# Kernel tuning notes

Hardware: AMD Instinct MI355X
Metric: run time of the kernel (lower is better)

Reference implementation:

```python
import jax, jax.numpy as jnp
import numpy as np

B, C, S = 256, 1024, 14   # batch, channels, spatial (frozen by y.view(b,c,14,14))
C2 = 15                   # channels2 in the module
CAT = C // 2 * 3 + C2     # 1551 = 15 + 512 + 1024
EPS = 1e-5


def _conv(x, w, b, groups, pad):
    out = jax.lax.conv_general_dilated(
        x, w, window_strides=(1, 1), padding=((pad, pad), (pad, pad)),
        dimension_numbers=('NCHW', 'OIHW', 'NCHW'), feature_group_count=groups)
    return out + b[None, :, None, None]


def _bn(x, gamma, beta):
    # training-mode BatchNorm2d: biased batch stats over (N,H,W)
    m = x.mean((0, 2, 3), keepdims=True)
    v = x.var((0, 2, 3), keepdims=True)
    return (x - m) * jax.lax.rsqrt(v + EPS) * gamma[None, :, None, None] + beta[None, :, None, None]


def setup_inputs() -> dict:
    key = jax.random.key(0)
    ks = jax.random.split(key, 16)
    r = C2 // 7  # = 2
    inp = {
        'y': jax.random.normal(ks[0], (B, C2, S * S), jnp.float32),
        'x': jax.random.normal(ks[1], (B, C, S, S), jnp.float32),
        'fc1_w': jax.random.normal(ks[2], (r, C2), jnp.float32) * 0.2,
        'fc2_w': jax.random.normal(ks[3], (C2, r), jnp.float32) * 0.2,
        'conv_w': jax.random.normal(ks[4], (C // 2, C, 1, 1), jnp.float32) * 0.03,
        'conv_b': jnp.zeros((C // 2,), jnp.float32),
        'dconv_w': jax.random.normal(ks[5], (C, 1, 3, 3), jnp.float32) * 0.2,
        'dconv_b': jnp.zeros((C,), jnp.float32),
        'dw1_w': jax.random.normal(ks[6], (CAT, 1, 3, 3), jnp.float32) * 0.2,
        'dw1_b': jnp.zeros((CAT,), jnp.float32),
        'pw1_w': jax.random.normal(ks[7], (C // 2, CAT, 1, 1), jnp.float32) * 0.03,
        'pw1_b': jnp.zeros((C // 2,), jnp.float32),
        'gamma': jnp.ones((C // 2,), jnp.float32),
        'beta': jnp.zeros((C // 2,), jnp.float32),
        'n': 0,
    }
    return inp


def reference(y, x, fc1_w, fc2_w, conv_w, conv_b, dconv_w, dconv_b,
              dw1_w, dw1_b, pw1_w, pw1_b, gamma, beta, n):
    b = y.shape[0]
    y4 = y.reshape(b, C2, S, S)
    # SE block on the 15 sub-channels
    g = y4.mean((2, 3))                              # (b, 15) global avg pool
    h = jax.nn.relu(g @ fc1_w.T) @ fc2_w.T           # (b, 15)
    y1 = y4 * jax.nn.sigmoid(h)[:, :, None, None]
    # depthwise conv on x, then per-(b,c) row covariance of the 14x14 map
    x1 = _conv(x, dconv_w, dconv_b, C, 1)            # (b, C, 14, 14)
    x2 = jax.lax.stop_gradient(x1)                   # .detach() in the original
    xc = x2 - x2.mean(-1, keepdims=True)             # np.cov: rows=vars, cols=obs
    cov = jnp.einsum('bcik,bcjk->bcij', xc, xc) / (S - 1)
    z = _conv(cov, conv_w, conv_b, 1, 0)             # 1x1 conv C -> C//2
    z = jax.nn.sigmoid(_bn(z, gamma, beta))
    for _ in range(n):                               # n=0 at these shapes
        y1 = jax.image.resize(y1, (y1.shape[0], y1.shape[1], y1.shape[2] * 2, y1.shape[3] * 2), 'bilinear')
    cat = jnp.concatenate([y1, z, x], axis=1)        # (b, 1551, 14, 14)
    o = _conv(cat, dw1_w, dw1_b, CAT, 1)             # depthwise 3x3
    o = _conv(o, pw1_w, pw1_b, 1, 0)                 # pointwise 1x1 -> C//2
    return jax.nn.relu(_bn(o, gamma, beta))
```

## Files before the change

### kernel.cpp

```cpp
#include <hip/hip_runtime.h>

typedef unsigned int u32;
typedef unsigned short u16;
typedef __attribute__((ext_vector_type(8))) short bf16x8;
typedef __attribute__((ext_vector_type(4))) float f32x4;
typedef __attribute__((ext_vector_type(4))) u32 u32x4;

#define EPSBN 1e-5f

#define GLDS16(gp, lp) __builtin_amdgcn_global_load_lds( \
    (const __attribute__((address_space(1))) u32*)(gp), \
    (__attribute__((address_space(3))) u32*)(lp), 16, 0, 0)

#define OFF_ADW    0ull
#define OFF_COVT   0ull
#define OFF_S      160563200ull
#define OFF_WBZ    160578560ull
#define OFF_WBP    161627136ull
#define OFF_STATSZ 163265536ull
#define OFF_STATSO 163269632ull
#define OFF_SCZ    163273728ull
#define OFF_SHZ    163275776ull
#define OFF_SCO    163277824ull
#define OFF_SHO    163279872ull

static __device__ __forceinline__ float bf2f(u16 h){
  u32 u = ((u32)h) << 16; float f; __builtin_memcpy(&f, &u, 4); return f;
}
static __device__ __forceinline__ u16 f2bf(float f){
  u32 u; __builtin_memcpy(&u, &f, 4);
  u = (u + 0x7fffu + ((u >> 16) & 1u)) >> 16;
  return (u16)u;
}
static __device__ __forceinline__ u32 pk2bf(float lo, float hi){
  u32 r;
  asm("v_cvt_pk_bf16_f32 %0, %1, %2" : "=v"(r) : "v"(lo), "v"(hi));
  return r;
}

__global__ __launch_bounds__(64) void se_kernel(const float* __restrict__ y,
    const float* __restrict__ fc1, const float* __restrict__ fc2, float* __restrict__ sse){
  __shared__ float g[15];
  __shared__ float t[2];
  int b = blockIdx.x, l = threadIdx.x;
  for (int c = 0; c < 15; ++c){
    float p = 0.f;
    for (int k = l; k < 196; k += 64) p += y[((size_t)b*15 + c)*196 + k];
    p += __shfl_xor(p, 32); p += __shfl_xor(p, 16); p += __shfl_xor(p, 8);
    p += __shfl_xor(p, 4);  p += __shfl_xor(p, 2);  p += __shfl_xor(p, 1);
    if (l == 0) g[c] = p * (1.f/196.f);
  }
  __syncthreads();
  if (l < 2){
    float a = 0.f;
    for (int c = 0; c < 15; ++c) a += g[c] * fc1[l*15 + c];
    t[l] = fmaxf(a, 0.f);
  }
  __syncthreads();
  if (l < 15){
    float h = t[0]*fc2[l*2] + t[1]*fc2[l*2+1];
    sse[b*15 + l] = 1.f / (1.f + __expf(-h));
  }
}

__global__ void wconv_kernel(const float* __restrict__ cw, const float* __restrict__ pw,
                             u16* __restrict__ wbz, u16* __restrict__ wbp){
  u32 stride = gridDim.x * blockDim.x;
  for (u32 i = blockIdx.x*blockDim.x + threadIdx.x; i < 524288u; i += stride)
    wbz[i] = f2bf(cw[i]);
  for (u32 i = blockIdx.x*blockDim.x + threadIdx.x; i < 819200u; i += stride){
    u32 n = i / 1600u, k = i - n*1600u;
    wbp[i] = f2bf(k < 1551u ? pw[(size_t)n*1551 + k] : 0.f);
  }
}

__global__ __launch_bounds__(256,2) void cov_kernel(const float* __restrict__ x,
    const float* __restrict__ dcw, const float* __restrict__ dcb, u16* __restrict__ covT){
  __shared__ __align__(16) float xs[2*3136];
  __shared__ __align__(16) u32 xcb[16*132];
  __shared__ __align__(16) u32 covL32[32*210];
  __shared__ float wls[64][9];
  __shared__ float wlb[64];

  int tid = threadIdx.x;
  int c0 = blockIdx.x * 64, b = blockIdx.y;
  const float* xbase = x + ((size_t)b*1024 + c0)*196;

  #pragma unroll
  for (int i = 0; i < 3; ++i){
    int s = tid + i*256;
    GLDS16(xbase + s*4, xs + s*4);
  }
  if (tid < 16){ int s = tid + 768; GLDS16(xbase + s*4, xs + s*4); }

  for (int i = tid; i < 576; i += 256) wls[i/9][i%9] = dcw[(size_t)(c0 + i/9)*9 + (i%9)];
  if (tid < 64) wlb[tid] = dcb[c0 + tid];

  for (int sg = 0; sg < 4; ++sg){
    u32 xo = (u32)(sg & 1) * 3136u;
    asm volatile("s_waitcnt vmcnt(0)" ::: "memory");
    __builtin_amdgcn_s_barrier();
    asm volatile("" ::: "memory");

    {
      int c = tid >> 4, i = tid & 15;
      int cg = sg*16 + c;
      u32 q[8];
      #pragma unroll
      for (int j = 0; j < 8; ++j) q[j] = 0u;
      if (i < 14){
        float wr[9];
        #pragma unroll
        for (int qq = 0; qq < 9; ++qq) wr[qq] = wls[cg][qq];
        float topm = (i > 0) ? 1.f : 0.f, botm = (i < 13) ? 1.f : 0.f;
        wr[0] *= topm; wr[1] *= topm; wr[2] *= topm;
        wr[6] *= botm; wr[7] *= botm; wr[8] *= botm;
        float bb = wlb[cg];
        float rr[3][16];
        #pragma unroll
        for (int d = 0; d < 3; ++d){
          rr[d][0] = 0.f; rr[d][15] = 0.f;
          int rowr = i + d - 1;
          rowr = rowr < 0 ? 0 : (rowr > 13 ? 13 : rowr);
          const float* src = &xs[xo + c*196 + rowr*14];
          #pragma unroll
          for (int j = 0; j < 7; ++j)
            *(float2*)&rr[d][1 + 2*j] = *(const float2*)&src[2*j];
        }
        float ov[14];
        #pragma unroll
        for (int k = 0; k < 14; ++k){
          float a = bb;
          #pragma unroll
          for (int dy = 0; dy < 3; ++dy)
            #pragma unroll
            for (int dx = 0; dx < 3; ++dx)
              a += wr[dy*3+dx] * rr[dy][k + dx];
          ov[k] = a;
        }
        float mean = 0.f;
        #pragma unroll
        for (int k = 0; k < 14; ++k) mean += ov[k];
        mean *= (1.f/14.f);
        #pragma unroll
        for (int j = 0; j < 7; ++j)
          q[j] = pk2bf(ov[2*j] - mean, ov[2*j+1] - mean);
      }
      u32x4 q0 = {q[0], q[1], q[2], q[3]};
      u32x4 q1 = {q[4], q[5], q[6], q[7]};
      *(u32x4*)&xcb[c*132 + i*8]     = q0;
      *(u32x4*)&xcb[c*132 + i*8 + 4] = q1;
    }
    __builtin_amdgcn_s_barrier();
    if (sg < 3){
      const float* nsrc = xbase + (size_t)(sg+1)*3136;
      u32 xo2 = xo ^ 3136u;
      #pragma unroll
      for (int i = 0; i < 3; ++i){
        int s = tid + i*256;
        GLDS16(nsrc + s*4, xs + xo2 + s*4);
      }
      if (tid < 16){ int s = tid + 768; GLDS16(nsrc + s*4, xs + xo2 + s*4); }
    }

    {
      int w = tid >> 6, l = tid & 63, lr = l & 15, lq = l >> 4;
      #pragma unroll
      for (int pp = 0; pp < 2; ++pp){
        int clo = w*4 + 2*pp;
        bf16x8 alo = {0,0,0,0,0,0,0,0}, ahi = {0,0,0,0,0,0,0,0};
        if (lq < 2){
          alo = *(const bf16x8*)&xcb[clo*132 + lr*8 + lq*4];
          ahi = *(const bf16x8*)&xcb[(clo+1)*132 + lr*8 + lq*4];
        }
        f32x4 dlo = {0.f,0.f,0.f,0.f}, dhi = {0.f,0.f,0.f,0.f};
        dlo = __builtin_amdgcn_mfma_f32_16x16x32_bf16(alo, alo, dlo, 0, 0, 0);
        dhi = __builtin_amdgcn_mfma_f32_16x16x32_bf16(ahi, ahi, dhi, 0, 0, 0);
        if (lr < 14){
          int cp = sg*8 + w*2 + pp;
          #pragma unroll
          for (int r = 0; r < 4; ++r){
            int rowi = lq*4 + r;
            if (rowi < 14){
              u32 vv = pk2bf(dlo[r] * (1.f/13.f), dhi[r] * (1.f/13.f));
              covL32[cp*210 + rowi*14 + lr] = vv;
            }
          }
        }
      }
    }
  }
  __syncthreads();

  for (int i = tid; i < 1568; i += 256){
    int g = i & 7, ij = i >> 3;
    u32x4 v;
    v.x = covL32[(g*4+0)*210 + ij];
    v.y = covL32[(g*4+1)*210 + ij];
    v.z = covL32[(g*4+2)*210 + ij];
    v.w = covL32[(g*4+3)*210 + ij];
    *(u32x4*)(covT + ((size_t)(b*196 + ij)*1024 + c0 + g*8)) = v;
  }
}

__global__ __launch_bounds__(256,5) void adw_kernel(
    const float* __restrict__ y, const float* __restrict__ sse,
    const u16* __restrict__ zT, const float* __restrict__ scz, const float* __restrict__ shz,
    const float* __restrict__ x, const float* __restrict__ dw1w, const float* __restrict__ dw1b,
    u16* __restrict__ Adw){
  __shared__ __align__(16) float ms[32*202];
  __shared__ float wd[32][9];
  __shared__ float bd[32];
  int tid = threadIdx.x;
  int cc0 = blockIdx.x * 32, b = blockIdx.y;

  for (int i = tid; i < 288; i += 256){
    int c = i / 9, q = i - c*9;
    int cc = cc0 + c;
    wd[c][q] = (cc < 1551) ? dw1w[(size_t)cc*9 + q] : 0.f;
  }
  if (tid < 32) bd[tid] = (cc0 + tid < 1551) ? dw1b[cc0 + tid] : 0.f;

  if (cc0 < 15){
    int ny = 15;
    for (int i = tid; i < ny*196; i += 256){
      u32 c = (u32)i / 196u, p = (u32)i - c*196u;
      ms[c*202u + p] = y[((size_t)b*15 + c)*196 + p] * sse[b*15 + c];
    }
  }
  {
    int zs = cc0 > 15 ? cc0 : 15;
    int ze = cc0 + 32 < 527 ? cc0 + 32 : 527;
    if (zs < ze){
      int nz = ze - zs, lbase = zs - cc0, obase = zs - 15;
      const u16* zrow = zT + (size_t)obase*50176 + (size_t)b*196;
      for (int i = tid; i < nz*98; i += 256){
        u32 oo = (u32)i / 98u, pp = (u32)i - oo*98u;
        u32 v = *(const u32*)(zrow + (size_t)oo*50176 + pp*2u);
        int o = obase + (int)oo;
        float s = scz[o], h = shz[o];
        float v0 = bf2f((u16)(v & 0xffffu)) * s + h;
        float v1 = bf2f((u16)(v >> 16))     * s + h;
        v0 = 1.f / (1.f + __expf(-v0));
        v1 = 1.f / (1.f + __expf(-v1));
        float2 fv = {v0, v1};
        *(float2*)&ms[(u32)(lbase + (int)oo)*202u + pp*2u] = fv;
      }
    }
  }
  {
    int xs_ = cc0 > 527 ? cc0 : 527;
    int xe = cc0 + 32 < 1551 ? cc0 + 32 : 1551;
    if (xs_ < xe){
      int nx = xe - xs_, lbase = xs_ - cc0, cxs = xs_ - 527;
      const float4* xg = (const float4*)(x + ((size_t)b*1024 + cxs)*196);
      for (int i = tid; i < nx*49; i += 256){
        float4 v = xg[i];
        u32 c = (u32)i / 49u, p4 = (u32)i - c*49u;
        float* dst = &ms[(u32)(lbase + (int)c)*202u + p4*4u];
        float2 lo = {v.x, v.y}, hi = {v.z, v.w};
        *(float2*)dst = lo;
        *(float2*)(dst + 2) = hi;
      }
    }
  }
  {
    int ps = cc0 > 1551 ? cc0 : 1551;
    int pe = cc0 + 32;
    if (ps < pe){
      int np = pe - ps, lbase = ps - cc0;
      for (int i = tid; i < np*196; i += 256){
        u32 c = (u32)i / 196u, p = (u32)i - c*196u;
        ms[(u32)(lbase + (int)c)*202u + p] = 0.f;
      }
    }
  }
  __syncthreads();

  for (int t = tid; t < 448; t += 256){
    int cc = t & 31, i = t >> 5;
    float wr[9];
    #pragma unroll
    for (int qq = 0; qq < 9; ++qq) wr[qq] = wd[cc][qq];
    float topm = (i > 0) ? 1.f : 0.f, botm = (i < 13) ? 1.f : 0.f;
    wr[0] *= topm; wr[1] *= topm; wr[2] *= topm;
    wr[6] *= botm; wr[7] *= botm; wr[8] *= botm;
    float bb = bd[cc];
    float rr[3][16];
    #pragma unroll
    for (int d = 0; d < 3; ++d){
      rr[d][0] = 0.f; rr[d][15] = 0.f;
      int rowr = i + d - 1;
      rowr = rowr < 0 ? 0 : (rowr > 13 ? 13 : rowr);
      const float* src = &ms[cc*202 + rowr*14];
      #pragma unroll
      for (int j = 0; j < 7; ++j)
        *(float2*)&rr[d][1 + 2*j] = *(const float2*)&src[2*j];
    }
    size_t obase = ((size_t)b*196 + i*14) * 1600 + cc0 + cc;
    #pragma unroll
    for (int k = 0; k < 14; ++k){
      float a = bb;
      #pragma unroll
      for (int dy = 0; dy < 3; ++dy)
        #pragma unroll
        for (int dx = 0; dx < 3; ++dx)
          a += wr[dy*3+dx] * rr[dy][k + dx];
      Adw[obase + (size_t)k*1600] = f2bf(a);
    }
  }
}

template<int MODE>
__global__ __launch_bounds__(256,2) void gemm_kernel(
    const u16* __restrict__ A, const u16* __restrict__ Bw,
    const float* __restrict__ bias, void* __restrict__ outp,
    float* __restrict__ stats, int K){
  __shared__ __align__(16) u16 lds[32768];

  int tid = threadIdx.x;
  int w = tid >> 6, l = tid & 63;
  int wm = w >> 1, wn = w & 1;
  int lr = l & 15, lq = l >> 4;
  u32 g = blockIdx.x;
  u32 lin = (g & 7u) * 196u + (g >> 3);
  int n0 = (int)(lin & 3u) * 128;
  int m0 = (int)(lin >> 2) * 128;

  f32x4 acc[4][4] = {};
  int kTiles = K >> 6;

  const u16* Abase = A  + (size_t)m0*K;
  const u16* Bbase = Bw + (size_t)n0*K;

  #pragma unroll
  for (int i = 0; i < 4; ++i){
    int s = tid + i*256;
    int row = s >> 3, c8 = s & 7, sc = c8 ^ (row & 7);
    GLDS16(Abase + (size_t)row*K + sc*8, lds + s*8);
    GLDS16(Bbase + (size_t)row*K + sc*8, lds + 8192 + s*8);
  }

  for (int kt = 0; kt < kTiles; ++kt){
    u32 bufo = (u32)(kt & 1) * 16384u;
    if (kt > 0) __builtin_amdgcn_s_barrier();
    if (kt + 1 < kTiles){
      u32 nbufo = bufo ^ 16384u;
      #pragma unroll
      for (int i = 0; i < 4; ++i){
        int s = tid + i*256;
        int row = s >> 3, c8 = s & 7, sc = c8 ^ (row & 7);
        GLDS16(Abase + (size_t)row*K + (kt+1)*64 + sc*8, lds + nbufo + s*8);
        GLDS16(Bbase + (size_t)row*K + (kt+1)*64 + sc*8, lds + nbufo + 8192 + s*8);
      }
      asm volatile("s_waitcnt vmcnt(8)" ::: "memory");
    } else {
      asm volatile("s_waitcnt vmcnt(0)" ::: "memory");
    }
    __builtin_amdgcn_s_barrier();
    asm volatile("" ::: "memory");
    const u16* Ac = lds + bufo;
    const u16* Bc = lds + bufo + 8192;
    #pragma unroll
    for (int ks = 0; ks < 2; ++ks){
      bf16x8 af[4], bfv[4];
      #pragma unroll
      for (int mi = 0; mi < 4; ++mi){
        int row = wm*64 + mi*16 + lr;
        int q = (ks*4 + lq) ^ (row & 7);
        af[mi] = *(const bf16x8*)(Ac + row*64 + q*8);
      }
      #pragma unroll
      for (int ni = 0; ni < 4; ++ni){
        int row = wn*64 + ni*16 + lr;
        int q = (ks*4 + lq) ^ (row & 7);
        bfv[ni] = *(const bf16x8*)(Bc + row*64 + q*8);
      }
      #pragma unroll
      for (int mi = 0; mi < 4; ++mi)
        #pragma unroll
        for (int ni = 0; ni < 4; ++ni)
          acc[mi][ni] = __builtin_amdgcn_mfma_f32_16x16x32_bf16(af[mi], bfv[ni], acc[mi][ni], 0, 0, 0);
    }
  }
  __syncthreads();

  #pragma unroll
  for (int ni = 0; ni < 4; ++ni){
    int col = n0 + wn*64 + ni*16 + lr;
    float bb = bias[col];
    float s1 = 0.f, s2 = 0.f;
    #pragma unroll
    for (int mi = 0; mi < 4; ++mi)
      #pragma unroll
      for (int r = 0; r < 4; ++r){
        float v = acc[mi][ni][r] + bb;
        acc[mi][ni][r] = v;
        s1 += v; s2 += v*v;
      }
    s1 += __shfl_xor(s1, 16); s1 += __shfl_xor(s1, 32);
    s2 += __shfl_xor(s2, 16); s2 += __shfl_xor(s2, 32);
    if (lq == 0){
      atomicAdd(&stats[col], s1);
      atomicAdd(&stats[512 + col], s2);
    }
  }

  float* eb = (float*)lds;
  #pragma unroll
  for (int rnd = 0; rnd < 2; ++rnd){
    if (wm == rnd){
      float* e = eb + wn * (64*65);
      #pragma unroll
      for (int mi = 0; mi < 4; ++mi)
        #pragma unroll
        for (int ni = 0; ni < 4; ++ni)
          #pragma unroll
          for (int r = 0; r < 4; ++r)
            e[(mi*16 + lq*4 + r)*65 + ni*16 + lr] = acc[mi][ni][r];
      int m = m0 + wm*64 + l;
      if (MODE == 0){
        u16* ob = (u16*)outp + (size_t)(n0 + wn*64)*50176 + m;
        #pragma unroll 8
        for (int no = 0; no < 64; ++no)
          ob[(size_t)no*50176] = f2bf(e[l*65 + no]);
      } else {
        u32 bq = (u32)m / 196u;
        u32 ij = (u32)m - bq*196u;
        float* ob = (float*)outp + ((size_t)bq*512 + n0 + wn*64)*196 + ij;
        #pragma unroll 8
        for (int no = 0; no < 64; ++no)
          ob[(size_t)no*196] = e[l*65 + no];
      }
    }
    __syncthreads();
  }
}

__global__ void bnprep_kernel(const float* __restrict__ stats, const float* __restrict__ gamma,
    const float* __restrict__ beta, float* __restrict__ sc, float* __restrict__ sh){
  int o = threadIdx.x;
  float m = stats[o] * (1.f/50176.f);
  float v = stats[512+o] * (1.f/50176.f) - m*m;
  float inv = rsqrtf(v + EPSBN);
  float g = gamma[o] * inv;
  sc[o] = g;
  sh[o] = beta[o] - m*g;
}

__global__ void final_kernel(float4* __restrict__ o4, const float* __restrict__ sc,
                             const float* __restrict__ sh){
  u32 stride = gridDim.x * blockDim.x;
  for (u32 i = blockIdx.x*blockDim.x + threadIdx.x; i < 6422528u; i += stride){
    u32 oc = (i / 49u) & 511u;
    float s = sc[oc], t = sh[oc];
    float4 v = o4[i];
    v.x = fmaxf(fmaf(v.x, s, t), 0.f);
    v.y = fmaxf(fmaf(v.y, s, t), 0.f);
    v.z = fmaxf(fmaf(v.z, s, t), 0.f);
    v.w = fmaxf(fmaf(v.w, s, t), 0.f);
    o4[i] = v;
  }
}

extern "C" void kernel_launch(void* const* d_in, const int* in_sizes, int n_in,
                              void* d_out, int out_size, void* d_ws, size_t ws_size,
                              hipStream_t stream){
  (void)in_sizes; (void)n_in; (void)out_size; (void)ws_size;
  const float* y      = (const float*)d_in[0];
  const float* x      = (const float*)d_in[1];
  const float* fc1    = (const float*)d_in[2];
  const float* fc2    = (const float*)d_in[3];
  const float* convw  = (const float*)d_in[4];
  const float* convb  = (const float*)d_in[5];
  const float* dconvw = (const float*)d_in[6];
  const float* dconvb = (const float*)d_in[7];
  const float* dw1w   = (const float*)d_in[8];
  const float* dw1b   = (const float*)d_in[9];
  const float* pw1w   = (const float*)d_in[10];
  const float* pw1b   = (const float*)d_in[11];
  const float* gamma  = (const float*)d_in[12];
  const float* beta   = (const float*)d_in[13];

  char* ws = (char*)d_ws;
  u16* covT   = (u16*)(ws + OFF_COVT);
  u16* Adw    = (u16*)(ws + OFF_ADW);
  float* sse  = (float*)(ws + OFF_S);
  u16* wbz    = (u16*)(ws + OFF_WBZ);
  u16* wbp    = (u16*)(ws + OFF_WBP);
  float* statsZ = (float*)(ws + OFF_STATSZ);
  float* statsO = (float*)(ws + OFF_STATSO);
  float* scz  = (float*)(ws + OFF_SCZ);
  float* shz  = (float*)(ws + OFF_SHZ);
  float* sco  = (float*)(ws + OFF_SCO);
  float* sho  = (float*)(ws + OFF_SHO);
  u16* zT     = (u16*)d_out;
  float* outf = (float*)d_out;

  hipMemsetAsync(statsZ, 0, 8192, stream);
  se_kernel<<<256, 64, 0, stream>>>(y, fc1, fc2, sse);
  wconv_kernel<<<2048, 256, 0, stream>>>(convw, pw1w, wbz, wbp);
  cov_kernel<<<dim3(16, 256), 256, 0, stream>>>(x, dconvw, dconvb, covT);
  gemm_kernel<0><<<1568, 256, 0, stream>>>(covT, wbz, convb, (void*)zT, statsZ, 1024);
  bnprep_kernel<<<1, 512, 0, stream>>>(statsZ, gamma, beta, scz, shz);
  adw_kernel<<<dim3(50, 256), 256, 0, stream>>>(y, sse, zT, scz, shz, x, dw1w, dw1b, Adw);
  gemm_kernel<1><<<1568, 256, 0, stream>>>(Adw, wbp, pw1b, (void*)outf, statsO, 1600);
  bnprep_kernel<<<1, 512, 0, stream>>>(statsO, gamma, beta, sco, sho);
  final_kernel<<<8192, 256, 0, stream>>>((float4*)outf, sco, sho);
}
```

Baseline: 485.6 us.

## Exploit covariance symmetry: compute only upper-triangle entries through the z GEMM

Since each 14x14 covariance is symmetric, the cov kernel writes only the 105 upper-triangle entries per (b,c), and the first GEMM runs over M=256*105 instead of 256*196. The GEMM weights off-diagonal rows twice in the BatchNorm statistics so the batch mean and variance stay exact. The adw kernel expands the z output back to the full 14x14 map through a lookup table. This cuts the first GEMM's FLOPs and the covT/zT memory traffic by nearly half, in exchange for scalar u16 gathers in adw instead of paired loads, plus extra per-block table setup.

```diff
diff --git a/kernel.cpp b/kernel.cpp
--- a/kernel.cpp
+++ b/kernel.cpp
@@ -81,6 +81,7 @@
   __shared__ __align__(16) u32 covL32[32*210];
   __shared__ float wls[64][9];
   __shared__ float wlb[64];
+  __shared__ u16 tij[112];
 
   int tid = threadIdx.x;
   int c0 = blockIdx.x * 64, b = blockIdx.y;
@@ -95,6 +96,13 @@
 
   for (int i = tid; i < 576; i += 256) wls[i/9][i%9] = dcw[(size_t)(c0 + i/9)*9 + (i%9)];
   if (tid < 64) wlb[tid] = dcb[c0 + tid];
+  if (tid < 196){
+    int ii = tid / 14, jj = tid - ii*14;
+    if (ii <= jj){
+      int t = 13*ii - (ii*(ii-1))/2 + jj;
+      tij[t] = (u16)tid;
+    }
+  }
 
   for (int sg = 0; sg < 4; ++sg){
     u32 xo = (u32)(sg & 1) * 3136u;
@@ -192,14 +200,15 @@
   }
   __syncthreads();
 
-  for (int i = tid; i < 1568; i += 256){
-    int g = i & 7, ij = i >> 3;
+  for (int i = tid; i < 840; i += 256){
+    int g = i & 7, t = i >> 3;
+    int ij = tij[t];
     u32x4 v;
     v.x = covL32[(g*4+0)*210 + ij];
     v.y = covL32[(g*4+1)*210 + ij];
     v.z = covL32[(g*4+2)*210 + ij];
     v.w = covL32[(g*4+3)*210 + ij];
-    *(u32x4*)(covT + ((size_t)(b*196 + ij)*1024 + c0 + g*8)) = v;
+    *(u32x4*)(covT + ((size_t)(b*105 + t)*1024 + c0 + g*8)) = v;
   }
 }
 
@@ -211,8 +220,16 @@
   __shared__ __align__(16) float ms[32*202];
   __shared__ float wd[32][9];
   __shared__ float bd[32];
+  __shared__ u16 ttab[196];
   int tid = threadIdx.x;
   int cc0 = blockIdx.x * 32, b = blockIdx.y;
+
+  if (tid < 196){
+    int ii = tid / 14, jj = tid - ii*14;
+    int im = ii < jj ? ii : jj, jm = ii < jj ? jj : ii;
+    ttab[tid] = (u16)(13*im - (im*(im-1))/2 + jm);
+  }
+  __syncthreads();
 
   for (int i = tid; i < 288; i += 256){
     int c = i / 9, q = i - c*9;
@@ -233,18 +250,14 @@
     int ze = cc0 + 32 < 527 ? cc0 + 32 : 527;
     if (zs < ze){
       int nz = ze - zs, lbase = zs - cc0, obase = zs - 15;
-      const u16* zrow = zT + (size_t)obase*50176 + (size_t)b*196;
-      for (int i = tid; i < nz*98; i += 256){
-        u32 oo = (u32)i / 98u, pp = (u32)i - oo*98u;
-        u32 v = *(const u32*)(zrow + (size_t)oo*50176 + pp*2u);
+      const u16* zb = zT + (size_t)obase*26880 + (size_t)b*105;
+      for (int i = tid; i < nz*196; i += 256){
+        u32 oo = (u32)i / 196u, p = (u32)i - oo*196u;
+        float v = bf2f(zb[(size_t)oo*26880 + ttab[p]]);
         int o = obase + (int)oo;
-        float s = scz[o], h = shz[o];
-        float v0 = bf2f((u16)(v & 0xffffu)) * s + h;
-        float v1 = bf2f((u16)(v >> 16))     * s + h;
-        v0 = 1.f / (1.f + __expf(-v0));
-        v1 = 1.f / (1.f + __expf(-v1));
-        float2 fv = {v0, v1};
-        *(float2*)&ms[(u32)(lbase + (int)oo)*202u + pp*2u] = fv;
+        v = v * scz[o] + shz[o];
+        v = 1.f / (1.f + __expf(-v));
+        ms[(u32)(lbase + (int)oo)*202u + p] = v;
       }
     }
   }
@@ -323,7 +336,8 @@
   int wm = w >> 1, wn = w & 1;
   int lr = l & 15, lq = l >> 4;
   u32 g = blockIdx.x;
-  u32 lin = (g & 7u) * 196u + (g >> 3);
+  u32 per = gridDim.x >> 3;
+  u32 lin = (g & 7u) * per + (g >> 3);
   int n0 = (int)(lin & 3u) * 128;
   int m0 = (int)(lin >> 2) * 128;
 
@@ -385,6 +399,27 @@
   }
   __syncthreads();
 
+  float wgt16[4][4];
+  if (MODE == 0){
+    float* wrow = (float*)lds + 8320;
+    for (int rb = tid; rb < 128; rb += 256){
+      u32 t = (u32)(m0 + rb) % 105u;
+      float wgt = 2.f;
+      #pragma unroll
+      for (int ii = 0; ii < 14; ++ii){
+        int td = 14*ii - (ii*(ii-1))/2;
+        if ((int)t == td) wgt = 1.f;
+      }
+      wrow[rb] = wgt;
+    }
+    __syncthreads();
+    #pragma unroll
+    for (int mi = 0; mi < 4; ++mi)
+      #pragma unroll
+      for (int r = 0; r < 4; ++r)
+        wgt16[mi][r] = wrow[wm*64 + mi*16 + lq*4 + r];
+  }
+
   #pragma unroll
   for (int ni = 0; ni < 4; ++ni){
     int col = n0 + wn*64 + ni*16 + lr;
@@ -396,7 +431,8 @@
       for (int r = 0; r < 4; ++r){
         float v = acc[mi][ni][r] + bb;
         acc[mi][ni][r] = v;
-        s1 += v; s2 += v*v;
+        float wv = (MODE == 0) ? wgt16[mi][r] : 1.f;
+        s1 += wv*v; s2 += wv*v*v;
       }
     s1 += __shfl_xor(s1, 16); s1 += __shfl_xor(s1, 32);
     s2 += __shfl_xor(s2, 16); s2 += __shfl_xor(s2, 32);
@@ -420,10 +456,10 @@
             e[(mi*16 + lq*4 + r)*65 + ni*16 + lr] = acc[mi][ni][r];
       int m = m0 + wm*64 + l;
       if (MODE == 0){
-        u16* ob = (u16*)outp + (size_t)(n0 + wn*64)*50176 + m;
+        u16* ob = (u16*)outp + (size_t)(n0 + wn*64)*26880 + m;
         #pragma unroll 8
         for (int no = 0; no < 64; ++no)
-          ob[(size_t)no*50176] = f2bf(e[l*65 + no]);
+          ob[(size_t)no*26880] = f2bf(e[l*65 + no]);
       } else {
         u32 bq = (u32)m / 196u;
         u32 ij = (u32)m - bq*196u;
@@ -501,7 +537,7 @@
   se_kernel<<<256, 64, 0, stream>>>(y, fc1, fc2, sse);
   wconv_kernel<<<2048, 256, 0, stream>>>(convw, pw1w, wbz, wbp);
   cov_kernel<<<dim3(16, 256), 256, 0, stream>>>(x, dconvw, dconvb, covT);
-  gemm_kernel<0><<<1568, 256, 0, stream>>>(covT, wbz, convb, (void*)zT, statsZ, 1024);
+  gemm_kernel<0><<<840, 256, 0, stream>>>(covT, wbz, convb, (void*)zT, statsZ, 1024);
   bnprep_kernel<<<1, 512, 0, stream>>>(statsZ, gamma, beta, scz, shz);
   adw_kernel<<<dim3(50, 256), 256, 0, stream>>>(y, sse, zT, scz, shz, x, dw1w, dw1b, Adw);
   gemm_kernel<1><<<1568, 256, 0, stream>>>(Adw, wbp, pw1b, (void*)outf, statsO, 1600);
```

New measurement: 474.6 us. 1.02x faster.
